# Optimization experiments

Hardware: AMD Instinct MI355X
Metric: run time of the kernel (lower is better)

## Reference

```python
import jax, jax.numpy as jnp
import numpy as np

RING_WORLD_SIZE = 4  # number of ring steps / KV sequence chunks


def _ring_flash_attention(q, k, v, ring_size):
    # q,k,v: [B, S, H, D]; non-causal full attention computed blockwise over
    # KV chunks (one per ring step) with numerically-stable online LSE merge,
    # mirroring _compact_ring_fwd + update_out_and_lse.
    B, S, H, D = q.shape
    scale = D ** (-0.5)
    chunk = S // ring_size
    out = None  # [B, S, H, D] accumulated in fp32
    lse = None  # [B, H, S] running log-sum-exp
    for step in range(ring_size):
        k_blk = jax.lax.dynamic_slice_in_dim(k, step * chunk, chunk, axis=1)
        v_blk = jax.lax.dynamic_slice_in_dim(v, step * chunk, chunk, axis=1)
        # scores: [B, H, Sq, Sk_blk]
        scores = jnp.einsum('bqhd,bkhd->bhqk', q, k_blk) * scale
        block_lse = jax.scipy.special.logsumexp(scores, axis=-1)  # [B,H,Sq]
        probs = jnp.exp(scores - block_lse[..., None])
        block_out = jnp.einsum('bhqk,bkhd->bqhd', probs, v_blk)
        if out is None:
            out, lse = block_out, block_lse
        else:
            new_lse = jnp.logaddexp(lse, block_lse)
            w_old = jnp.exp(lse - new_lse)       # [B,H,Sq]
            w_new = jnp.exp(block_lse - new_lse)
            # broadcast weights to [B,Sq,H,1]
            out = (jnp.transpose(w_old, (0, 2, 1))[..., None] * out
                   + jnp.transpose(w_new, (0, 2, 1))[..., None] * block_out)
            lse = new_lse
    return out.astype(q.dtype)


def setup_inputs() -> dict:
    key = jax.random.key(0)
    kq, kk, kv = jax.random.split(key, 3)
    shape = (1, 4096, 16, 128)
    return {
        'query': jax.random.normal(kq, shape, dtype=jnp.float32),
        'key': jax.random.normal(kk, shape, dtype=jnp.float32),
        'value': jax.random.normal(kv, shape, dtype=jnp.float32),
    }


def reference(query, key, value):
    # Ulysses all-to-all is identity on a single logical device; the ring loop
    # with lossless (error-feedback) KV compression reduces to blockwise
    # attention with online softmax merging.
    return _ring_flash_attention(query, key, value, RING_WORLD_SIZE)
```

## Files before the change

kernel.cpp:

```cpp
#include <hip/hip_runtime.h>
#include <hip/hip_bf16.h>

#define S_LEN 4096
#define NH    16
#define DD    128
#define HD    2048
#define QB    128
#define KB    64
#define NT    (S_LEN/KB)

typedef __bf16 bf16_t;
typedef bf16_t bf16x8 __attribute__((ext_vector_type(8)));
typedef float  f32x4  __attribute__((ext_vector_type(4)));

static __device__ __forceinline__ bf16x8 pack8(float4 a, float4 b, float s) {
  bf16x8 v;
  v[0]=(bf16_t)(a.x*s); v[1]=(bf16_t)(a.y*s); v[2]=(bf16_t)(a.z*s); v[3]=(bf16_t)(a.w*s);
  v[4]=(bf16_t)(b.x*s); v[5]=(bf16_t)(b.y*s); v[6]=(bf16_t)(b.z*s); v[7]=(bf16_t)(b.w*s);
  return v;
}

static __device__ __forceinline__ void gload_lds16(const void* g, void* l) {
  __builtin_amdgcn_global_load_lds((const __attribute__((address_space(1))) void*)g,
                                   (__attribute__((address_space(3))) void*)l, 16, 0, 0);
}

__global__ __launch_bounds__(256) void prep_k(const float* __restrict__ Kg,
                                              bf16_t* __restrict__ Kp) {
  const int kt = blockIdx.x, h = blockIdx.y, tid = threadIdx.x;
  __shared__ bf16_t tile[KB][DD + 8];
  #pragma unroll
  for (int it = 0; it < 8; ++it) {
    int lin4 = it*256 + tid;
    int r  = lin4 >> 5;
    int dc = (lin4 & 31) * 4;
    float4 a = *(const float4*)(Kg + (size_t)(kt*KB + r)*HD + h*DD + dc);
    tile[r][dc+0]=(bf16_t)a.x; tile[r][dc+1]=(bf16_t)a.y;
    tile[r][dc+2]=(bf16_t)a.z; tile[r][dc+3]=(bf16_t)a.w;
  }
  __syncthreads();
  bf16_t* out = Kp + (size_t)(h*NT + kt)*8192;
  #pragma unroll
  for (int it = 0; it < 4; ++it) {
    int cid = it*256 + tid;
    int f = cid >> 6, l = cid & 63;
    int b = f >> 2, c = f & 3;
    int row = b*16 + (l & 15);
    int d0  = c*32 + (l >> 4)*8;
    bf16x8 v = *(const bf16x8*)(&tile[row][d0]);
    *(bf16x8*)(out + (size_t)cid*8) = v;
  }
}

__global__ __launch_bounds__(256) void prep_v(const float* __restrict__ Vg,
                                              bf16_t* __restrict__ Vp) {
  const int kt = blockIdx.x, h = blockIdx.y, tid = threadIdx.x;
  __shared__ bf16_t tile[KB][DD + 8];
  #pragma unroll
  for (int it = 0; it < 8; ++it) {
    int lin4 = it*256 + tid;
    int r  = lin4 >> 5;
    int dc = (lin4 & 31) * 4;
    float4 a = *(const float4*)(Vg + (size_t)(kt*KB + r)*HD + h*DD + dc);
    tile[r][dc+0]=(bf16_t)a.x; tile[r][dc+1]=(bf16_t)a.y;
    tile[r][dc+2]=(bf16_t)a.z; tile[r][dc+3]=(bf16_t)a.w;
  }
  __syncthreads();
  bf16_t* out = Vp + (size_t)(h*NT + kt)*8192;
  #pragma unroll
  for (int it = 0; it < 4; ++it) {
    int cid = it*256 + tid;
    int f = cid >> 6, l = cid & 63;
    int ks = f >> 3, db = f & 7;
    int d  = db*16 + (l & 15);
    int c0 = ks*32 + (l >> 4)*8;
    bf16x8 v;
    #pragma unroll
    for (int m = 0; m < 8; ++m) {
      int c = c0 + m;
      int k = 32*(c>>5) + 16*((c>>2)&1) + 4*((c>>3)&3) + (c&3);
      v[m] = tile[k][d];
    }
    *(bf16x8*)(out + (size_t)cid*8) = v;
  }
}

#define QK_COMPUTE(DST, KSBASE)                                                  \
  do {                                                                           \
    _Pragma("unroll")                                                            \
    for (int b_ = 0; b_ < 4; ++b_) {                                             \
      _Pragma("unroll")                                                          \
      for (int c_ = 0; c_ < 4; ++c_) {                                           \
        bf16x8 kb_ = *(const bf16x8*)((KSBASE) + ((b_*4 + c_) << 10));           \
        DST[0][b_] = __builtin_amdgcn_mfma_f32_16x16x32_bf16(kb_, qf[0][c_], DST[0][b_], 0, 0, 0); \
        DST[1][b_] = __builtin_amdgcn_mfma_f32_16x16x32_bf16(kb_, qf[1][c_], DST[1][b_], 0, 0, 0); \
      }                                                                          \
    }                                                                            \
  } while (0)

#define SOFTMAX_PV(SC)                                                           \
  do {                                                                           \
    bf16x8 pp[2][2];                                                             \
    _Pragma("unroll")                                                            \
    for (int g = 0; g < 2; ++g) {                                                \
      float pmax;                                                                \
      {                                                                          \
        float a0 = fmaxf(fmaxf(SC[g][0][0], SC[g][0][1]), SC[g][0][2]);          \
        float a1 = fmaxf(fmaxf(SC[g][0][3], SC[g][1][0]), SC[g][1][1]);          \
        float a2 = fmaxf(fmaxf(SC[g][1][2], SC[g][1][3]), SC[g][2][0]);          \
        float a3 = fmaxf(fmaxf(SC[g][2][1], SC[g][2][2]), SC[g][2][3]);          \
        float a4 = fmaxf(fmaxf(SC[g][3][0], SC[g][3][1]), SC[g][3][2]);          \
        float b0 = fmaxf(fmaxf(a0, a1), a2);                                     \
        float b1 = fmaxf(fmaxf(a3, a4), SC[g][3][3]);                            \
        pmax = fmaxf(b0, b1);                                                    \
        pmax = fmaxf(pmax, __shfl_xor(pmax, 16));                                \
        pmax = fmaxf(pmax, __shfl_xor(pmax, 32));                                \
      }                                                                          \
      if (!__all(pmax - m_run[g] <= 8.0f)) {                                     \
        float mnew  = fmaxf(m_run[g], pmax);                                     \
        float alpha = exp2f(m_run[g] - mnew);                                    \
        m_run[g] = mnew;                                                         \
        _Pragma("unroll")                                                        \
        for (int i = 0; i < 8; ++i) {                                            \
          _Pragma("unroll")                                                      \
          for (int r = 0; r < 4; ++r) acc[g][i][r] *= alpha;                     \
        }                                                                        \
        _Pragma("unroll")                                                        \
        for (int r = 0; r < 4; ++r) acc_l[g][r] *= alpha;                        \
      }                                                                          \
      _Pragma("unroll")                                                          \
      for (int b_ = 0; b_ < 4; ++b_) {                                           \
        _Pragma("unroll")                                                        \
        for (int r = 0; r < 4; ++r) {                                            \
          float p = exp2f(SC[g][b_][r] - m_run[g]);                              \
          pp[g][b_ >> 1][(b_ & 1)*4 + r] = (bf16_t)p;                            \
        }                                                                        \
      }                                                                          \
    }                                                                            \
    __builtin_amdgcn_s_setprio(1);                                               \
    _Pragma("unroll")                                                            \
    for (int ks = 0; ks < 2; ++ks) {                                             \
      acc_l[0] = __builtin_amdgcn_mfma_f32_16x16x32_bf16(onesf, pp[0][ks], acc_l[0], 0, 0, 0); \
      acc_l[1] = __builtin_amdgcn_mfma_f32_16x16x32_bf16(onesf, pp[1][ks], acc_l[1], 0, 0, 0); \
      _Pragma("unroll")                                                          \
      for (int db = 0; db < 8; ++db) {                                           \
        bf16x8 va = vf[ks*8 + db];                                               \
        acc[0][db] = __builtin_amdgcn_mfma_f32_16x16x32_bf16(va, pp[0][ks], acc[0][db], 0, 0, 0); \
        acc[1][db] = __builtin_amdgcn_mfma_f32_16x16x32_bf16(va, pp[1][ks], acc[1][db], 0, 0, 0); \
      }                                                                          \
    }                                                                            \
    __builtin_amdgcn_s_setprio(0);                                               \
  } while (0)

__global__ __launch_bounds__(256, 2) void attn_fwd(const float* __restrict__ Qg,
                                                   const bf16_t* __restrict__ Kp,
                                                   const bf16_t* __restrict__ Vp,
                                                   float* __restrict__ Og) {
  const int phys = blockIdx.x;
  const int logical = (phys & 7) * 64 + (phys >> 3);
  const int h  = logical >> 5;
  const int qt = logical & 31;
  const int tid  = threadIdx.x;
  const int wid  = tid >> 6;
  const int lane = tid & 63;
  const int l16  = lane & 15;
  const int lg   = lane >> 4;
  const int lo16 = lane * 16;

  __shared__ alignas(16) bf16_t Ks[2][8192];
  __shared__ alignas(16) bf16_t Vt[2][8192];

  const float qs = 0.08838834764831845f * 1.4426950408889634f;
  bf16x8 qf[2][4];
  #pragma unroll
  for (int g = 0; g < 2; ++g) {
    const int qrow = qt*QB + wid*32 + g*16 + l16;
    const float* qp = Qg + (size_t)qrow*HD + h*DD + lg*8;
    #pragma unroll
    for (int c = 0; c < 4; ++c) {
      float4 a = *(const float4*)(qp + c*32);
      float4 b = *(const float4*)(qp + c*32 + 4);
      qf[g][c] = pack8(a, b, qs);
    }
  }
  bf16x8 onesf;
  #pragma unroll
  for (int j = 0; j < 8; ++j) onesf[j] = (bf16_t)1.0f;
  asm volatile("" ::: "memory");

  const int lo = tid*16;
  auto issue = [&](int kt) {
    int b = kt & 1;
    const char* kg = (const char*)(Kp + (size_t)(h*NT + kt)*8192);
    const char* vg = (const char*)(Vp + (size_t)(h*NT + kt)*8192);
    char* kl = (char*)&Ks[b][0];
    char* vl = (char*)&Vt[b][0];
    #pragma unroll
    for (int p = 0; p < 4; ++p) gload_lds16(kg + lo + p*4096, kl + lo + p*4096);
    #pragma unroll
    for (int p = 0; p < 4; ++p) gload_lds16(vg + lo + p*4096, vl + lo + p*4096);
  };

  f32x4 acc[2][8];
  f32x4 acc_l[2];
  #pragma unroll
  for (int g = 0; g < 2; ++g) {
    #pragma unroll
    for (int i = 0; i < 8; ++i) acc[g][i] = (f32x4){0.f,0.f,0.f,0.f};
    acc_l[g] = (f32x4){0.f,0.f,0.f,0.f};
  }
  float m_run[2] = {-__builtin_inff(), -__builtin_inff()};

  issue(0);
  issue(1);
  asm volatile("s_waitcnt vmcnt(8)" ::: "memory");
  __builtin_amdgcn_s_barrier();
  __builtin_amdgcn_sched_barrier(0);

  f32x4 sc[2][4];
  #pragma unroll
  for (int g = 0; g < 2; ++g)
    #pragma unroll
    for (int b = 0; b < 4; ++b) sc[g][b] = (f32x4){0.f,0.f,0.f,0.f};
  {
    const char* KsB = (const char*)&Ks[0][0] + lo16;
    QK_COMPUTE(sc, KsB);
  }

  for (int kt = 0; kt < NT-1; ++kt) {
    const int cur = kt & 1;
    bf16x8 vf[16];
    {
      const char* VtB = (const char*)&Vt[cur][0] + lo16;
      #pragma unroll
      for (int f = 0; f < 16; ++f) vf[f] = *(const bf16x8*)(VtB + (f << 10));
    }
    asm volatile("s_waitcnt lgkmcnt(0)" ::: "memory");
    __builtin_amdgcn_sched_barrier(0);
    __builtin_amdgcn_s_barrier();
    if (kt + 2 < NT) {
      issue(kt + 2);
      asm volatile("s_waitcnt vmcnt(8)" ::: "memory");
    } else {
      asm volatile("s_waitcnt vmcnt(0)" ::: "memory");
    }
    __builtin_amdgcn_s_barrier();
    __builtin_amdgcn_sched_barrier(0);

    f32x4 scn[2][4];
    #pragma unroll
    for (int g = 0; g < 2; ++g)
      #pragma unroll
      for (int b = 0; b < 4; ++b) scn[g][b] = (f32x4){0.f,0.f,0.f,0.f};
    {
      const char* KsB = (const char*)&Ks[cur ^ 1][0] + lo16;
      QK_COMPUTE(scn, KsB);
    }
    SOFTMAX_PV(sc);

    #pragma unroll
    for (int g = 0; g < 2; ++g)
      #pragma unroll
      for (int b = 0; b < 4; ++b) sc[g][b] = scn[g][b];
  }

  {
    bf16x8 vf[16];
    const char* VtB = (const char*)&Vt[(NT-1) & 1][0] + lo16;
    #pragma unroll
    for (int f = 0; f < 16; ++f) vf[f] = *(const bf16x8*)(VtB + (f << 10));
    SOFTMAX_PV(sc);
  }

  #pragma unroll
  for (int g = 0; g < 2; ++g) {
    const int qrow = qt*QB + wid*32 + g*16 + l16;
    const float inv = 1.0f / acc_l[g][0];
    float* op = Og + (size_t)qrow*HD + h*DD + lg*4;
    #pragma unroll
    for (int db = 0; db < 8; ++db) {
      float4 o;
      o.x = acc[g][db][0]*inv; o.y = acc[g][db][1]*inv;
      o.z = acc[g][db][2]*inv; o.w = acc[g][db][3]*inv;
      *(float4*)(op + db*16) = o;
    }
  }
}

extern "C" void kernel_launch(void* const* d_in, const int* in_sizes, int n_in,
                              void* d_out, int out_size, void* d_ws, size_t ws_size,
                              hipStream_t stream) {
  const float* Q = (const float*)d_in[0];
  const float* K = (const float*)d_in[1];
  const float* V = (const float*)d_in[2];
  float* O = (float*)d_out;
  bf16_t* Kp = (bf16_t*)d_ws;
  bf16_t* Vp = Kp + (size_t)NH*S_LEN*DD;
  prep_k<<<dim3(NT, NH), 256, 0, stream>>>(K, Kp);
  prep_v<<<dim3(NT, NH), 256, 0, stream>>>(V, Vp);
  attn_fwd<<<dim3(512), 256, 0, stream>>>(Q, Kp, Vp, O);
}
```

Before: 185.5 us.

## Use two waves per block with 64 query rows each and ping-pong score buffers

Blocks shrink from 4 waves of 32 query rows to 2 waves of 64 rows (128 threads, launch bound 1), so each K/V fragment read from LDS feeds four MFMA row groups instead of two. V fragments are now read from LDS directly inside the PV loop rather than preloaded into registers. The main loop is unrolled by two with alternating score buffers to avoid copying, and the barrier/prefetch structure is reordered so the next tile is issued after compute. Register pressure roughly doubles for accumulators and occupancy drops, which risks spills and less latency hiding.

```diff
diff --git a/kernel.cpp b/kernel.cpp
--- a/kernel.cpp
+++ b/kernel.cpp
@@ -88,21 +88,28 @@
 #define QK_COMPUTE(DST, KSBASE)                                                  \
   do {                                                                           \
     _Pragma("unroll")                                                            \
+    for (int g_ = 0; g_ < 4; ++g_)                                               \
+      _Pragma("unroll")                                                          \
+      for (int b_ = 0; b_ < 4; ++b_) DST[g_][b_] = (f32x4){0.f,0.f,0.f,0.f};     \
+    __builtin_amdgcn_s_setprio(1);                                               \
+    _Pragma("unroll")                                                            \
     for (int b_ = 0; b_ < 4; ++b_) {                                             \
       _Pragma("unroll")                                                          \
       for (int c_ = 0; c_ < 4; ++c_) {                                           \
         bf16x8 kb_ = *(const bf16x8*)((KSBASE) + ((b_*4 + c_) << 10));           \
-        DST[0][b_] = __builtin_amdgcn_mfma_f32_16x16x32_bf16(kb_, qf[0][c_], DST[0][b_], 0, 0, 0); \
-        DST[1][b_] = __builtin_amdgcn_mfma_f32_16x16x32_bf16(kb_, qf[1][c_], DST[1][b_], 0, 0, 0); \
-      }                                                                          \
-    }                                                                            \
+        _Pragma("unroll")                                                        \
+        for (int g_ = 0; g_ < 4; ++g_)                                           \
+          DST[g_][b_] = __builtin_amdgcn_mfma_f32_16x16x32_bf16(kb_, qf[g_][c_], DST[g_][b_], 0, 0, 0); \
+      }                                                                          \
+    }                                                                            \
+    __builtin_amdgcn_s_setprio(0);                                               \
   } while (0)
 
-#define SOFTMAX_PV(SC)                                                           \
+#define SOFTMAX_PV(SC, VTB)                                                      \
   do {                                                                           \
-    bf16x8 pp[2][2];                                                             \
-    _Pragma("unroll")                                                            \
-    for (int g = 0; g < 2; ++g) {                                                \
+    bf16x8 pp[4][2];                                                             \
+    _Pragma("unroll")                                                            \
+    for (int g = 0; g < 4; ++g) {                                                \
       float pmax;                                                                \
       {                                                                          \
         float a0 = fmaxf(fmaxf(SC[g][0][0], SC[g][0][1]), SC[g][0][2]);          \
@@ -140,19 +147,41 @@
     __builtin_amdgcn_s_setprio(1);                                               \
     _Pragma("unroll")                                                            \
     for (int ks = 0; ks < 2; ++ks) {                                             \
-      acc_l[0] = __builtin_amdgcn_mfma_f32_16x16x32_bf16(onesf, pp[0][ks], acc_l[0], 0, 0, 0); \
-      acc_l[1] = __builtin_amdgcn_mfma_f32_16x16x32_bf16(onesf, pp[1][ks], acc_l[1], 0, 0, 0); \
+      _Pragma("unroll")                                                          \
+      for (int g = 0; g < 4; ++g)                                                \
+        acc_l[g] = __builtin_amdgcn_mfma_f32_16x16x32_bf16(onesf, pp[g][ks], acc_l[g], 0, 0, 0); \
       _Pragma("unroll")                                                          \
       for (int db = 0; db < 8; ++db) {                                           \
-        bf16x8 va = vf[ks*8 + db];                                               \
-        acc[0][db] = __builtin_amdgcn_mfma_f32_16x16x32_bf16(va, pp[0][ks], acc[0][db], 0, 0, 0); \
-        acc[1][db] = __builtin_amdgcn_mfma_f32_16x16x32_bf16(va, pp[1][ks], acc[1][db], 0, 0, 0); \
+        bf16x8 va = *(const bf16x8*)((VTB) + ((ks*8 + db) << 10));               \
+        _Pragma("unroll")                                                        \
+        for (int g = 0; g < 4; ++g)                                              \
+          acc[g][db] = __builtin_amdgcn_mfma_f32_16x16x32_bf16(va, pp[g][ks], acc[g][db], 0, 0, 0); \
       }                                                                          \
     }                                                                            \
     __builtin_amdgcn_s_setprio(0);                                               \
   } while (0)
 
-__global__ __launch_bounds__(256, 2) void attn_fwd(const float* __restrict__ Qg,
+#define BODY(SCUR, SNXT, KT)                                                     \
+  do {                                                                           \
+    const int cur_ = (KT) & 1;                                                   \
+    asm volatile("s_waitcnt vmcnt(0)" ::: "memory");                             \
+    __builtin_amdgcn_s_barrier();                                                \
+    __builtin_amdgcn_sched_barrier(0);                                           \
+    {                                                                            \
+      const char* KsB_ = (const char*)&Ks[cur_ ^ 1][0] + lo16;                   \
+      QK_COMPUTE(SNXT, KsB_);                                                    \
+    }                                                                            \
+    {                                                                            \
+      const char* VtB_ = (const char*)&Vt[cur_][0] + lo16;                       \
+      SOFTMAX_PV(SCUR, VtB_);                                                    \
+    }                                                                            \
+    asm volatile("s_waitcnt lgkmcnt(0)" ::: "memory");                           \
+    __builtin_amdgcn_sched_barrier(0);                                           \
+    __builtin_amdgcn_s_barrier();                                                \
+    if ((KT) + 2 < NT) issue((KT) + 2);                                          \
+  } while (0)
+
+__global__ __launch_bounds__(128, 1) void attn_fwd(const float* __restrict__ Qg,
                                                    const bf16_t* __restrict__ Kp,
                                                    const bf16_t* __restrict__ Vp,
                                                    float* __restrict__ Og) {
@@ -171,10 +200,10 @@
   __shared__ alignas(16) bf16_t Vt[2][8192];
 
   const float qs = 0.08838834764831845f * 1.4426950408889634f;
-  bf16x8 qf[2][4];
-  #pragma unroll
-  for (int g = 0; g < 2; ++g) {
-    const int qrow = qt*QB + wid*32 + g*16 + l16;
+  bf16x8 qf[4][4];
+  #pragma unroll
+  for (int g = 0; g < 4; ++g) {
+    const int qrow = qt*QB + wid*64 + g*16 + l16;
     const float* qp = Qg + (size_t)qrow*HD + h*DD + lg*8;
     #pragma unroll
     for (int c = 0; c < 4; ++c) {
@@ -196,85 +225,47 @@
     char* kl = (char*)&Ks[b][0];
     char* vl = (char*)&Vt[b][0];
     #pragma unroll
-    for (int p = 0; p < 4; ++p) gload_lds16(kg + lo + p*4096, kl + lo + p*4096);
-    #pragma unroll
-    for (int p = 0; p < 4; ++p) gload_lds16(vg + lo + p*4096, vl + lo + p*4096);
+    for (int p = 0; p < 8; ++p) gload_lds16(kg + lo + p*2048, kl + lo + p*2048);
+    #pragma unroll
+    for (int p = 0; p < 8; ++p) gload_lds16(vg + lo + p*2048, vl + lo + p*2048);
   };
 
-  f32x4 acc[2][8];
-  f32x4 acc_l[2];
-  #pragma unroll
-  for (int g = 0; g < 2; ++g) {
+  f32x4 acc[4][8];
+  f32x4 acc_l[4];
+  #pragma unroll
+  for (int g = 0; g < 4; ++g) {
     #pragma unroll
     for (int i = 0; i < 8; ++i) acc[g][i] = (f32x4){0.f,0.f,0.f,0.f};
     acc_l[g] = (f32x4){0.f,0.f,0.f,0.f};
   }
-  float m_run[2] = {-__builtin_inff(), -__builtin_inff()};
+  float m_run[4] = {-__builtin_inff(), -__builtin_inff(), -__builtin_inff(), -__builtin_inff()};
 
   issue(0);
   issue(1);
-  asm volatile("s_waitcnt vmcnt(8)" ::: "memory");
+  asm volatile("s_waitcnt vmcnt(16)" ::: "memory");
   __builtin_amdgcn_s_barrier();
   __builtin_amdgcn_sched_barrier(0);
 
-  f32x4 sc[2][4];
-  #pragma unroll
-  for (int g = 0; g < 2; ++g)
-    #pragma unroll
-    for (int b = 0; b < 4; ++b) sc[g][b] = (f32x4){0.f,0.f,0.f,0.f};
+  f32x4 scA[4][4], scB[4][4];
   {
-    const char* KsB = (const char*)&Ks[0][0] + lo16;
-    QK_COMPUTE(sc, KsB);
-  }
-
-  for (int kt = 0; kt < NT-1; ++kt) {
-    const int cur = kt & 1;
-    bf16x8 vf[16];
-    {
-      const char* VtB = (const char*)&Vt[cur][0] + lo16;
-      #pragma unroll
-      for (int f = 0; f < 16; ++f) vf[f] = *(const bf16x8*)(VtB + (f << 10));
-    }
-    asm volatile("s_waitcnt lgkmcnt(0)" ::: "memory");
-    __builtin_amdgcn_sched_barrier(0);
-    __builtin_amdgcn_s_barrier();
-    if (kt + 2 < NT) {
-      issue(kt + 2);
-      asm volatile("s_waitcnt vmcnt(8)" ::: "memory");
-    } else {
-      asm volatile("s_waitcnt vmcnt(0)" ::: "memory");
-    }
-    __builtin_amdgcn_s_barrier();
-    __builtin_amdgcn_sched_barrier(0);
-
-    f32x4 scn[2][4];
-    #pragma unroll
-    for (int g = 0; g < 2; ++g)
-      #pragma unroll
-      for (int b = 0; b < 4; ++b) scn[g][b] = (f32x4){0.f,0.f,0.f,0.f};
-    {
-      const char* KsB = (const char*)&Ks[cur ^ 1][0] + lo16;
-      QK_COMPUTE(scn, KsB);
-    }
-    SOFTMAX_PV(sc);
-
-    #pragma unroll
-    for (int g = 0; g < 2; ++g)
-      #pragma unroll
-      for (int b = 0; b < 4; ++b) sc[g][b] = scn[g][b];
-  }
+    const char* KsB_ = (const char*)&Ks[0][0] + lo16;
+    QK_COMPUTE(scA, KsB_);
+  }
+
+  for (int kt = 0; kt < NT-2; kt += 2) {
+    BODY(scA, scB, kt);
+    BODY(scB, scA, kt+1);
+  }
+  BODY(scA, scB, NT-2);
 
   {
-    bf16x8 vf[16];
-    const char* VtB = (const char*)&Vt[(NT-1) & 1][0] + lo16;
-    #pragma unroll
-    for (int f = 0; f < 16; ++f) vf[f] = *(const bf16x8*)(VtB + (f << 10));
-    SOFTMAX_PV(sc);
-  }
-
-  #pragma unroll
-  for (int g = 0; g < 2; ++g) {
-    const int qrow = qt*QB + wid*32 + g*16 + l16;
+    const char* VtB_ = (const char*)&Vt[(NT-1) & 1][0] + lo16;
+    SOFTMAX_PV(scB, VtB_);
+  }
+
+  #pragma unroll
+  for (int g = 0; g < 4; ++g) {
+    const int qrow = qt*QB + wid*64 + g*16 + l16;
     const float inv = 1.0f / acc_l[g][0];
     float* op = Og + (size_t)qrow*HD + h*DD + lg*4;
     #pragma unroll
@@ -298,5 +289,5 @@
   bf16_t* Vp = Kp + (size_t)NH*S_LEN*DD;
   prep_k<<<dim3(NT, NH), 256, 0, stream>>>(K, Kp);
   prep_v<<<dim3(NT, NH), 256, 0, stream>>>(V, Vp);
-  attn_fwd<<<dim3(512), 256, 0, stream>>>(Q, Kp, Vp, O);
-}
+  attn_fwd<<<dim3(512), 128, 0, stream>>>(Q, Kp, Vp, O);
+}
```

Measured after the change: 322.7 us. +73.9%, slower.
